# Performance work log

Hardware: AMD Instinct MI355X
Metric: run time of the kernel (lower is better)

## Reference

```python
import jax, jax.numpy as jnp
import numpy as np
from jax import lax

B, T, C_IN, H, K = 8, 4096, 256, 256, 3


def _conv1d_same(x_nct, w_oik, b_o):
    # x: [B, C, T], w: [H, C, K], b: [H] -> [B, H, T], 'same' padding
    y = lax.conv_general_dilated(x_nct, w_oik, window_strides=(1,),
                                 padding='SAME',
                                 dimension_numbers=('NCH', 'OIH', 'NCH'))
    return y + b_o[None, :, None]


def setup_inputs() -> dict:
    key = jax.random.key(0)
    ks = jax.random.split(key, 7)
    std = 1.0 / np.sqrt(H)
    u = lambda k, shape: jax.random.uniform(k, shape, jnp.float32, -std, std)
    return {
        'inputs': jax.random.normal(ks[0], (B, T, C_IN), jnp.float32),
        'init_f': jax.random.normal(ks[1], (B, H), jnp.float32),
        'init_z': jax.random.normal(ks[2], (B, H), jnp.float32),
        'f_w': u(ks[3], (H, C_IN, K)),
        'f_b': u(ks[4], (H,)),
        'z_w': u(ks[5], (H, C_IN, K)),
        'z_b': u(ks[6], (H,)),
    }


def reference(inputs, init_f, init_z, f_w, f_b, z_w, z_b):
    x = jnp.transpose(inputs, (0, 2, 1))                    # [B, C, T]
    raw_f = jnp.transpose(_conv1d_same(x, f_w, f_b), (0, 2, 1))  # [B, T, H]
    raw_z = jnp.transpose(_conv1d_same(x, z_w, z_b), (0, 2, 1))
    # prepend init state along time: init_state[0] -> f, init_state[1] -> z
    raw_f = jnp.concatenate([init_f[:, None, :], raw_f], axis=1)  # [B, T+1, H]
    raw_z = jnp.concatenate([init_z[:, None, :], raw_z], axis=1)
    log_one_minus_f = jax.nn.log_sigmoid(-raw_f)
    log_z = jax.nn.log_sigmoid(raw_z)
    log_f = jax.nn.log_sigmoid(raw_f)
    cs = jnp.cumsum(log_f, axis=1)
    recurrent_gates = log_f - cs + cs[:, -1:, :]
    log_hidden = lax.cumlogsumexp(log_z + log_one_minus_f + recurrent_gates, axis=1)
    return jnp.exp(log_hidden - recurrent_gates)            # [B, T+1, H]
```

## Files before the change

kernel.cpp:

```cpp
#include <hip/hip_runtime.h>
#include <hip/hip_bf16.h>

#define B_ 8
#define T_ 4096
#define C_ 256
#define H_ 256
#define K_ 3
#define NC 128
#define TC 32
#define WFRAG_ELEMS (24 * 32 * 64 * 8)

typedef __attribute__((ext_vector_type(8))) __bf16 bf16x8;
typedef __attribute__((ext_vector_type(4))) float f32x4;

__device__ __forceinline__ float sigm(float x) { return 1.0f / (1.0f + __expf(-x)); }

__device__ __forceinline__ ushort f2bf(float f) {
    union { float f; unsigned u; } v; v.f = f;
    return (ushort)((v.u + 0x7FFFu + ((v.u >> 16) & 1u)) >> 16);
}
__device__ __forceinline__ float bf2f(ushort u) {
    union { unsigned u; float f; } v; v.u = ((unsigned)u) << 16; return v.f;
}
__device__ __forceinline__ unsigned cvt_pk_bf16(float lo, float hi) {
    unsigned r;
    asm("v_cvt_pk_bf16_f32 %0, %1, %2" : "=v"(r) : "v"(lo), "v"(hi));
    return r;
}

__global__ __launch_bounds__(256) void wfrag_kernel(const float* __restrict__ fw,
                                                    const float* __restrict__ zw,
                                                    ushort* __restrict__ wfrag) {
    int idx = blockIdx.x * 256 + threadIdx.x;
    if (idx >= WFRAG_ELEMS) return;
    int j   = idx & 7;
    int l   = (idx >> 3) & 63;
    int ntg = (idx >> 9) & 31;
    int ks  = idx >> 14;
    int n = ntg * 16 + (l & 15);
    int kappa = ks * 32 + (l >> 4) * 8 + j;
    int k = kappa >> 8, c = kappa & 255;
    const float* w = (n < 256) ? fw : zw;
    int h = n & 255;
    wfrag[idx] = f2bf(w[(h * C_ + c) * K_ + k]);
}

__device__ __forceinline__ void bload(const ushort* wb, int ks, const int (&ntg)[4],
                                      bf16x8 (&dst)[4]) {
#pragma unroll
    for (int ni = 0; ni < 4; ++ni)
        dst[ni] = *(const bf16x8*)(wb + (size_t)ks * 16384 + (size_t)ntg[ni] * 512);
}

__device__ __forceinline__ void conv_step(const char* smem, int ks, int lr, int lg,
                                          const bf16x8 (&bfr)[4], f32x4 (&acc)[4][4]) {
    const int k = ks >> 3;
    const int cb = ((ks & 7) * 32 + lg * 8) * 2;
    bf16x8 afr[4];
#pragma unroll
    for (int mi = 0; mi < 4; ++mi) {
        int row = mi * 16 + lr + k;
        afr[mi] = *(const bf16x8*)(smem + row * 512 + (cb ^ ((row & 7) << 4)));
    }
#pragma unroll
    for (int ni = 0; ni < 4; ++ni)
#pragma unroll
        for (int mi = 0; mi < 4; ++mi)
            acc[mi][ni] = __builtin_amdgcn_mfma_f32_16x16x32_bf16(afr[mi], bfr[ni], acc[mi][ni], 0, 0, 0);
}

__global__ __launch_bounds__(512, 4) void conv_scan_kernel(const float* __restrict__ x,
                                                           const ushort* __restrict__ wfrag,
                                                           const float* __restrict__ fb,
                                                           const float* __restrict__ zb,
                                                           unsigned* __restrict__ AP,
                                                           unsigned* __restrict__ APl,
                                                           float* __restrict__ fl) {
    __shared__ __align__(16) char smem[65536];
    unsigned* buf = (unsigned*)smem;

    const int b = blockIdx.y;
    const int t0 = blockIdx.x * 64;
    const int tid = threadIdx.x;

    if (blockIdx.x == 0 || blockIdx.x == gridDim.x - 1) {
        for (int idx = tid; idx < 66 * 64; idx += 512) {
            int row = idx >> 6;
            int c4 = (idx & 63) * 4;
            int t = t0 - 1 + row;
            float4 v = make_float4(0.f, 0.f, 0.f, 0.f);
            if (t >= 0 && t < T_) v = *(const float4*)(x + ((size_t)(b * T_ + t)) * C_ + c4);
            uint2 w2 = make_uint2(cvt_pk_bf16(v.x, v.y), cvt_pk_bf16(v.z, v.w));
            *(uint2*)(smem + row * 512 + ((c4 * 2) ^ ((row & 7) << 4))) = w2;
        }
    } else {
        for (int idx = tid; idx < 66 * 64; idx += 512) {
            int row = idx >> 6;
            int c4 = (idx & 63) * 4;
            int t = t0 - 1 + row;
            float4 v = *(const float4*)(x + ((size_t)(b * T_ + t)) * C_ + c4);
            uint2 w2 = make_uint2(cvt_pk_bf16(v.x, v.y), cvt_pk_bf16(v.z, v.w));
            *(uint2*)(smem + row * 512 + ((c4 * 2) ^ ((row & 7) << 4))) = w2;
        }
    }
    __syncthreads();

    const int wv = tid >> 6;
    const int l  = tid & 63;
    const int lr = l & 15;
    const int lg = l >> 4;
    const int h0 = wv * 32;

    f32x4 acc[4][4];
#pragma unroll
    for (int ni = 0; ni < 4; ++ni) {
        float bv = (ni < 2 ? fb : zb)[h0 + (ni & 1) * 16 + lr];
        f32x4 bvv = {bv, bv, bv, bv};
#pragma unroll
        for (int mi = 0; mi < 4; ++mi) acc[mi][ni] = bvv;
    }

    const ushort* wb = wfrag + (size_t)l * 8;
    int ntg_[4];
#pragma unroll
    for (int ni = 0; ni < 4; ++ni)
        ntg_[ni] = (ni < 2) ? (wv * 2 + ni) : (16 + wv * 2 + ni - 2);

    bf16x8 ba[4], bb[4];
    bload(wb, 0, ntg_, ba);
#pragma unroll 1
    for (int ks = 0; ks < 24; ks += 2) {
        bload(wb, ks + 1, ntg_, bb);
        conv_step(smem, ks, lr, lg, ba, acc);
        if (ks + 2 < 24) bload(wb, ks + 2, ntg_, ba);
        conv_step(smem, ks + 1, lr, lg, bb, acc);
    }

    __syncthreads();
#pragma unroll
    for (int mi = 0; mi < 4; ++mi) {
#pragma unroll
        for (int ni = 0; ni < 2; ++ni) {
            const int h = h0 + ni * 16 + lr;
#pragma unroll
            for (int r = 0; r < 4; ++r) {
                float fv = sigm(acc[mi][ni][r]);
                float av = sigm(acc[mi][ni + 2][r]) * (1.0f - fv);
                int tl = (mi & 1) * 16 + lg * 4 + r;
                int trow = (mi >> 1) * 32 + tl;
                buf[trow * 256 + (h ^ ((tl << 2) & 31))] = cvt_pk_bf16(av, fv);
            }
        }
    }
    __syncthreads();

    {
        const int ch = tid >> 8;
        const int h = tid & 255;
        const int chunk = blockIdx.x * 2 + ch;
        const int r0 = chunk * TC;
        const unsigned* bp = buf + ch * 32 * 256;
        unsigned* app = AP + ((size_t)b * T_ + r0) * H_ + h;
        unsigned u = bp[h];
        float A = bf2f((ushort)(u & 0xffff));
        float Pp = 1.0f;
        float f_prev = bf2f((ushort)(u >> 16));
        unsigned upk = cvt_pk_bf16(A, Pp);
        app[0] = upk;
#pragma unroll 8
        for (int j = 1; j < TC; ++j) {
            u = bp[j * 256 + (h ^ ((j << 2) & 31))];
            float a = bf2f((ushort)(u & 0xffff));
            float f = bf2f((ushort)(u >> 16));
            A = fmaf(f_prev, A, a);
            Pp *= f_prev;
            f_prev = f;
            upk = cvt_pk_bf16(A, Pp);
            app[(size_t)j * H_] = upk;
        }
        APl[((size_t)b * NC + chunk) * H_ + h] = upk;
        fl[((size_t)b * NC + chunk) * H_ + h] = f_prev;
    }
}

__global__ __launch_bounds__(256) void combine_kernel(const unsigned* __restrict__ APl,
                                                      const float* __restrict__ fl,
                                                      const float* __restrict__ init_f,
                                                      const float* __restrict__ init_z,
                                                      float* __restrict__ out,
                                                      float* __restrict__ sin_) {
    const int b = blockIdx.x;
    const int h = threadIdx.x;
    float f0 = sigm(init_f[b * H_ + h]);
    float z0 = sigm(init_z[b * H_ + h]);
    float s = z0 * (1.0f - f0);
    out[(size_t)b * (T_ + 1) * H_ + h] = s;
    float flp = f0;
    const unsigned* ap = APl + (size_t)b * NC * H_ + h;
    const float* fp = fl + (size_t)b * NC * H_ + h;
    float* sp = sin_ + (size_t)b * NC * H_ + h;
#pragma unroll 8
    for (int c = 0; c < NC; ++c) {
        unsigned u = ap[(size_t)c * H_];
        float fln = fp[(size_t)c * H_];
        float st = flp * s;
        sp[(size_t)c * H_] = st;
        s = fmaf(bf2f((ushort)(u >> 16)), st, bf2f((ushort)(u & 0xffff)));
        flp = fln;
    }
}

__global__ __launch_bounds__(256) void apply_kernel(const unsigned* __restrict__ AP,
                                                    const float* __restrict__ sin_,
                                                    float* __restrict__ out) {
    const int c = blockIdx.x;
    const int b = blockIdx.y;
    const int tid = threadIdx.x;
    const int jr = tid >> 6;
    const int h4 = (tid & 63) * 4;
    const int r0 = c * TC;
    const float4 s4 = *(const float4*)(sin_ + ((size_t)b * NC + c) * H_ + h4);
#pragma unroll
    for (int p = 0; p < 8; ++p) {
        const int j = p * 4 + jr;
        const uint4 u4 = *(const uint4*)(AP + ((size_t)b * T_ + r0 + j) * H_ + h4);
        float4 o;
        o.x = fmaf(bf2f((ushort)(u4.x >> 16)), s4.x, bf2f((ushort)(u4.x & 0xffff)));
        o.y = fmaf(bf2f((ushort)(u4.y >> 16)), s4.y, bf2f((ushort)(u4.y & 0xffff)));
        o.z = fmaf(bf2f((ushort)(u4.z >> 16)), s4.z, bf2f((ushort)(u4.z & 0xffff)));
        o.w = fmaf(bf2f((ushort)(u4.w >> 16)), s4.w, bf2f((ushort)(u4.w & 0xffff)));
        *(float4*)(out + ((size_t)b * (T_ + 1) + r0 + 1 + j) * H_ + h4) = o;
    }
}

extern "C" void kernel_launch(void* const* d_in, const int* in_sizes, int n_in,
                              void* d_out, int out_size, void* d_ws, size_t ws_size,
                              hipStream_t stream) {
    const float* inputs = (const float*)d_in[0];
    const float* init_f = (const float*)d_in[1];
    const float* init_z = (const float*)d_in[2];
    const float* f_w    = (const float*)d_in[3];
    const float* f_b    = (const float*)d_in[4];
    const float* z_w    = (const float*)d_in[5];
    const float* z_b    = (const float*)d_in[6];
    float* out = (float*)d_out;

    ushort* wfrag = (ushort*)d_ws;
    unsigned* AP  = (unsigned*)(wfrag + WFRAG_ELEMS);
    unsigned* APl = AP + (size_t)B_ * T_ * H_;
    float* fl     = (float*)(APl + (size_t)B_ * NC * H_);
    float* sin_   = fl + (size_t)B_ * NC * H_;

    wfrag_kernel<<<(WFRAG_ELEMS + 255) / 256, 256, 0, stream>>>(f_w, z_w, wfrag);

    dim3 cgrid(T_ / 64, B_, 1);
    conv_scan_kernel<<<cgrid, 512, 0, stream>>>(inputs, wfrag, f_b, z_b, AP, APl, fl);

    combine_kernel<<<B_, H_, 0, stream>>>(APl, fl, init_f, init_z, out, sin_);

    dim3 agrid(NC, B_, 1);
    apply_kernel<<<agrid, 256, 0, stream>>>(AP, sin_, out);
}
```

Measured before the change: 66.19 us.

## Fuse chunk-carry combine into apply kernel with redundant per-block prefix

Drops the serial combine kernel, which ran on only 8 blocks. Each apply block now recomputes the carry-in for its chunk by folding the per-chunk affine pairs (f*A, f*P) stored by the scan kernel, then applies the carry to its 32 rows. This removes one launch and the serialized 128-step chain on a tiny grid. In exchange it adds redundant work that grows with chunk index, up to 128 dependent loads for the last chunks. The apply stores also become scalar per-thread instead of float4.

```diff
diff --git a/kernel.cpp b/kernel.cpp
--- a/kernel.cpp
+++ b/kernel.cpp
@@ -74,8 +74,7 @@
                                                            const float* __restrict__ fb,
                                                            const float* __restrict__ zb,
                                                            unsigned* __restrict__ AP,
-                                                           unsigned* __restrict__ APl,
-                                                           float* __restrict__ fl) {
+                                                           float2* __restrict__ ab) {
     __shared__ __align__(16) char smem[65536];
     unsigned* buf = (unsigned*)smem;
 
@@ -165,8 +164,7 @@
         float A = bf2f((ushort)(u & 0xffff));
         float Pp = 1.0f;
         float f_prev = bf2f((ushort)(u >> 16));
-        unsigned upk = cvt_pk_bf16(A, Pp);
-        app[0] = upk;
+        app[0] = cvt_pk_bf16(A, Pp);
 #pragma unroll 8
         for (int j = 1; j < TC; ++j) {
             u = bp[j * 256 + (h ^ ((j << 2) & 31))];
@@ -175,61 +173,40 @@
             A = fmaf(f_prev, A, a);
             Pp *= f_prev;
             f_prev = f;
-            upk = cvt_pk_bf16(A, Pp);
-            app[(size_t)j * H_] = upk;
-        }
-        APl[((size_t)b * NC + chunk) * H_ + h] = upk;
-        fl[((size_t)b * NC + chunk) * H_ + h] = f_prev;
-    }
-}
-
-__global__ __launch_bounds__(256) void combine_kernel(const unsigned* __restrict__ APl,
-                                                      const float* __restrict__ fl,
-                                                      const float* __restrict__ init_f,
-                                                      const float* __restrict__ init_z,
-                                                      float* __restrict__ out,
-                                                      float* __restrict__ sin_) {
-    const int b = blockIdx.x;
+            app[(size_t)j * H_] = cvt_pk_bf16(A, Pp);
+        }
+        ab[((size_t)b * NC + chunk) * H_ + h] = make_float2(f_prev * A, f_prev * Pp);
+    }
+}
+
+__global__ __launch_bounds__(256) void chainapply_kernel(const unsigned* __restrict__ AP,
+                                                         const float2* __restrict__ ab,
+                                                         const float* __restrict__ init_f,
+                                                         const float* __restrict__ init_z,
+                                                         float* __restrict__ out) {
+    const int c = blockIdx.x;
+    const int b = blockIdx.y;
     const int h = threadIdx.x;
+
     float f0 = sigm(init_f[b * H_ + h]);
     float z0 = sigm(init_z[b * H_ + h]);
-    float s = z0 * (1.0f - f0);
-    out[(size_t)b * (T_ + 1) * H_ + h] = s;
-    float flp = f0;
-    const unsigned* ap = APl + (size_t)b * NC * H_ + h;
-    const float* fp = fl + (size_t)b * NC * H_ + h;
-    float* sp = sin_ + (size_t)b * NC * H_ + h;
+    float s0 = z0 * (1.0f - f0);
+    if (c == 0) out[(size_t)b * (T_ + 1) * H_ + h] = s0;
+
+    float uv = f0 * s0;
+    const float2* abp = ab + (size_t)b * NC * H_ + h;
 #pragma unroll 8
-    for (int c = 0; c < NC; ++c) {
-        unsigned u = ap[(size_t)c * H_];
-        float fln = fp[(size_t)c * H_];
-        float st = flp * s;
-        sp[(size_t)c * H_] = st;
-        s = fmaf(bf2f((ushort)(u >> 16)), st, bf2f((ushort)(u & 0xffff)));
-        flp = fln;
-    }
-}
-
-__global__ __launch_bounds__(256) void apply_kernel(const unsigned* __restrict__ AP,
-                                                    const float* __restrict__ sin_,
-                                                    float* __restrict__ out) {
-    const int c = blockIdx.x;
-    const int b = blockIdx.y;
-    const int tid = threadIdx.x;
-    const int jr = tid >> 6;
-    const int h4 = (tid & 63) * 4;
-    const int r0 = c * TC;
-    const float4 s4 = *(const float4*)(sin_ + ((size_t)b * NC + c) * H_ + h4);
-#pragma unroll
-    for (int p = 0; p < 8; ++p) {
-        const int j = p * 4 + jr;
-        const uint4 u4 = *(const uint4*)(AP + ((size_t)b * T_ + r0 + j) * H_ + h4);
-        float4 o;
-        o.x = fmaf(bf2f((ushort)(u4.x >> 16)), s4.x, bf2f((ushort)(u4.x & 0xffff)));
-        o.y = fmaf(bf2f((ushort)(u4.y >> 16)), s4.y, bf2f((ushort)(u4.y & 0xffff)));
-        o.z = fmaf(bf2f((ushort)(u4.z >> 16)), s4.z, bf2f((ushort)(u4.z & 0xffff)));
-        o.w = fmaf(bf2f((ushort)(u4.w >> 16)), s4.w, bf2f((ushort)(u4.w & 0xffff)));
-        *(float4*)(out + ((size_t)b * (T_ + 1) + r0 + 1 + j) * H_ + h4) = o;
+    for (int cc = 0; cc < c; ++cc) {
+        float2 q = abp[(size_t)cc * H_];
+        uv = fmaf(q.y, uv, q.x);
+    }
+
+    const unsigned* app = AP + ((size_t)b * T_ + c * TC) * H_ + h;
+    float* op = out + ((size_t)b * (T_ + 1) + c * TC + 1) * H_ + h;
+#pragma unroll 8
+    for (int j = 0; j < TC; ++j) {
+        unsigned w = app[(size_t)j * H_];
+        op[(size_t)j * H_] = fmaf(bf2f((ushort)(w >> 16)), uv, bf2f((ushort)(w & 0xffff)));
     }
 }
 
@@ -247,17 +224,13 @@
 
     ushort* wfrag = (ushort*)d_ws;
     unsigned* AP  = (unsigned*)(wfrag + WFRAG_ELEMS);
-    unsigned* APl = AP + (size_t)B_ * T_ * H_;
-    float* fl     = (float*)(APl + (size_t)B_ * NC * H_);
-    float* sin_   = fl + (size_t)B_ * NC * H_;
+    float2* ab    = (float2*)(AP + (size_t)B_ * T_ * H_);
 
     wfrag_kernel<<<(WFRAG_ELEMS + 255) / 256, 256, 0, stream>>>(f_w, z_w, wfrag);
 
     dim3 cgrid(T_ / 64, B_, 1);
-    conv_scan_kernel<<<cgrid, 512, 0, stream>>>(inputs, wfrag, f_b, z_b, AP, APl, fl);
-
-    combine_kernel<<<B_, H_, 0, stream>>>(APl, fl, init_f, init_z, out, sin_);
+    conv_scan_kernel<<<cgrid, 512, 0, stream>>>(inputs, wfrag, f_b, z_b, AP, ab);
 
     dim3 agrid(NC, B_, 1);
-    apply_kernel<<<agrid, 256, 0, stream>>>(AP, sin_, out);
-}
+    chainapply_kernel<<<agrid, 256, 0, stream>>>(AP, ab, init_f, init_z, out);
+}
```

After: 65.14 us. Within noise of the previous version (-1.6%).
